# Kernel optimization log

Hardware: AMD Instinct MI355X
Metric: run time of the kernel (lower is better)

The kernel has to match this reference:

```python
import jax, jax.numpy as jnp
import numpy as np

EPS = 1e-6

def _ln(x):
    m = jnp.mean(x, -1, keepdims=True)
    v = jnp.mean((x - m) ** 2, -1, keepdims=True)
    return (x - m) * jax.lax.rsqrt(v + EPS)

def _rms(x, w):
    return x * jax.lax.rsqrt(jnp.mean(x * x, -1, keepdims=True) + EPS) * w

def _rotate_half(x):
    xr = x.reshape(x.shape[:-1] + (-1, 2))
    return jnp.stack([-xr[..., 1], xr[..., 0]], axis=-1).reshape(x.shape)

def _rope(x, cos, sin):
    # x: [B,L,H,D]; cos/sin: [L,D] interleaved-duplicated per pair
    c = cos[None, :, None, :]
    s = sin[None, :, None, :]
    return x * c + _rotate_half(x) * s

def _modulate(x, shift, scale):
    return x * (1.0 + scale[:, None, :]) + shift[:, None, :]

def _gate(x, g):
    return x * g[:, None, :]

def setup_inputs() -> dict:
    key = jax.random.key(0)
    ks = jax.random.split(key, 20)
    B, LI, LT, D, NH, HD, M = 1, 2048, 256, 2048, 16, 128, 8192
    def n(k, shape, s=1.0):
        return jax.random.normal(k, shape, dtype=jnp.float32) * s
    theta = jax.random.uniform(ks[0], (LI, HD // 2), dtype=jnp.float32) * 6.2831853
    freqs_cos = jnp.repeat(jnp.cos(theta), 2, axis=-1)  # [LI, HD]
    freqs_sin = jnp.repeat(jnp.sin(theta), 2, axis=-1)
    inp = {
        'img': n(ks[1], (B, LI, D)),
        'txt': n(ks[2], (B, LT, D)),
        'vec': n(ks[3], (B, D)),
        'freqs_cos': freqs_cos,
        'freqs_sin': freqs_sin,
        'attn_mask': jnp.ones((B, LI + LT), dtype=bool),
        # img stream params
        'img_mod_w': n(ks[4], (D, 6 * D), 0.02), 'img_mod_b': jnp.zeros((6 * D,), jnp.float32),
        'img_qkv_w': n(ks[5], (D, 3 * D), 0.02),
        'img_qn_w': jnp.ones((HD,), jnp.float32), 'img_kn_w': jnp.ones((HD,), jnp.float32),
        'img_proj_w': n(ks[6], (D, D), 0.02),
        'img_fc1_w': n(ks[7], (D, M), 0.02), 'img_fc1_b': jnp.zeros((M,), jnp.float32),
        'img_fc2_w': n(ks[8], (M, D), 0.02), 'img_fc2_b': jnp.zeros((D,), jnp.float32),
        # txt stream params
        'txt_mod_w': n(ks[9], (D, 6 * D), 0.02), 'txt_mod_b': jnp.zeros((6 * D,), jnp.float32),
        'txt_qkv_w': n(ks[10], (D, 3 * D), 0.02),
        'txt_qn_w': jnp.ones((HD,), jnp.float32), 'txt_kn_w': jnp.ones((HD,), jnp.float32),
        'txt_proj_w': n(ks[11], (D, D), 0.02),
        'txt_fc1_w': n(ks[12], (D, M), 0.02), 'txt_fc1_b': jnp.zeros((M,), jnp.float32),
        'txt_fc2_w': n(ks[13], (M, D), 0.02), 'txt_fc2_b': jnp.zeros((D,), jnp.float32),
    }
    return inp

def reference(img, txt, vec, freqs_cos, freqs_sin, attn_mask,
              img_mod_w, img_mod_b, img_qkv_w, img_qn_w, img_kn_w, img_proj_w,
              img_fc1_w, img_fc1_b, img_fc2_w, img_fc2_b,
              txt_mod_w, txt_mod_b, txt_qkv_w, txt_qn_w, txt_kn_w, txt_proj_w,
              txt_fc1_w, txt_fc1_b, txt_fc2_w, txt_fc2_b):
    B, LI, D = img.shape
    LT = txt.shape[1]
    HD = img_qn_w.shape[0]
    NH = D // HD
    vec_s = jax.nn.silu(vec)
    im = vec_s @ img_mod_w + img_mod_b
    i_s1, i_sc1, i_g1, i_s2, i_sc2, i_g2 = jnp.split(im, 6, axis=-1)
    tm = vec_s @ txt_mod_w + txt_mod_b
    t_s1, t_sc1, t_g1, t_s2, t_sc2, t_g2 = jnp.split(tm, 6, axis=-1)
    # img pre-attention
    ix = _modulate(_ln(img), i_s1, i_sc1)
    iqkv = (ix @ img_qkv_w).reshape(B, LI, 3, NH, HD)
    iq = _rms(iqkv[:, :, 0], img_qn_w)
    ik = _rms(iqkv[:, :, 1], img_kn_w)
    iv = iqkv[:, :, 2]
    iq = _rope(iq, freqs_cos, freqs_sin)
    ik = _rope(ik, freqs_cos, freqs_sin)
    # txt pre-attention (no rope)
    tx = _modulate(_ln(txt), t_s1, t_sc1)
    tqkv = (tx @ txt_qkv_w).reshape(B, LT, 3, NH, HD)
    tq = _rms(tqkv[:, :, 0], txt_qn_w)
    tk = _rms(tqkv[:, :, 1], txt_kn_w)
    tv = tqkv[:, :, 2]
    # joint attention over concat(img, txt)
    q = jnp.concatenate([iq, tq], axis=1)  # [B,S,H,D]
    k = jnp.concatenate([ik, tk], axis=1)
    v = jnp.concatenate([iv, tv], axis=1)
    scores = jnp.einsum('bqhd,bkhd->bhqk', q, k) / jnp.sqrt(jnp.float32(HD))
    scores = jnp.where(attn_mask[:, None, None, :], scores, jnp.float32(-1e30))
    p = jax.nn.softmax(scores, axis=-1)
    attn = jnp.einsum('bhqk,bkhd->bqhd', p, v).reshape(B, LI + LT, D)
    img_attn, txt_attn = attn[:, :LI], attn[:, LI:]
    # img residual branches
    img = img + _gate(img_attn @ img_proj_w, i_g1)
    h = _modulate(_ln(img), i_s2, i_sc2)
    h = jax.nn.gelu(h @ img_fc1_w + img_fc1_b, approximate=True) @ img_fc2_w + img_fc2_b
    img = img + _gate(h, i_g2)
    # txt residual branches
    txt = txt + _gate(txt_attn @ txt_proj_w, t_g1)
    h = _modulate(_ln(txt), t_s2, t_sc2)
    h = jax.nn.gelu(h @ txt_fc1_w + txt_fc1_b, approximate=True) @ txt_fc2_w + txt_fc2_b
    txt = txt + _gate(h, t_g2)
    return (img, txt)
```

## Files before the change

### kernel.cpp

```cpp
#include <hip/hip_runtime.h>
#include <hip/hip_bf16.h>
#include <cstdint>
#include <cstddef>

typedef __bf16 bf16x8 __attribute__((ext_vector_type(8)));
typedef float  f32x4  __attribute__((ext_vector_type(4)));
typedef __hip_bfloat16 hbf16;

#define DEVI static __device__ __forceinline__

DEVI unsigned short f2bf_bits(float x){
  hbf16 h = __float2bfloat16(x);
  return *reinterpret_cast<unsigned short*>(&h);
}
DEVI float gelu_tanh(float x){
  float u = x*(1.0f + 0.044715f*x*x);
  float t = exp2f(-2.3022119f*u);
  return x/(1.0f+t);
}

typedef __attribute__((address_space(1))) const unsigned int* gas_p;
typedef __attribute__((address_space(3))) unsigned int* las_p;
DEVI void gload16(const void* g, void* l){
  __builtin_amdgcn_global_load_lds((gas_p)g, (las_p)l, 16, 0, 0);
}


__global__ void silu_k(const float* __restrict__ v, float* __restrict__ o, int n){
  int i = blockIdx.x*blockDim.x + threadIdx.x;
  if (i < n){ float x = v[i]; o[i] = x/(1.0f+__expf(-x)); }
}

__global__ __launch_bounds__(256) void mod_part_k(const float* __restrict__ vs,
                                                  const float* __restrict__ W,
                                                  float* __restrict__ part){
  int j  = blockIdx.x*1024 + threadIdx.x*4;
  int i0 = blockIdx.y*64;
  float4 acc = {0.f,0.f,0.f,0.f};
  for (int i=0;i<64;i++){
    float s = vs[i0+i];
    float4 w = *(const float4*)(W + (size_t)(i0+i)*12288 + j);
    acc.x += s*w.x; acc.y += s*w.y; acc.z += s*w.z; acc.w += s*w.w;
  }
  *(float4*)(part + (size_t)blockIdx.y*12288 + j) = acc;
}

__global__ __launch_bounds__(256) void mod_red_k(const float* __restrict__ part,
                                                 const float* __restrict__ b,
                                                 float* __restrict__ out){
  int j = blockIdx.x*1024 + threadIdx.x*4;
  float4 acc = *(const float4*)(b + j);
  #pragma unroll
  for (int y=0;y<32;y++){
    float4 p = *(const float4*)(part + (size_t)y*12288 + j);
    acc.x += p.x; acc.y += p.y; acc.z += p.z; acc.w += p.w;
  }
  *(float4*)(out + j) = acc;
}

__global__ __launch_bounds__(256) void ln_mod_k(
    const float* __restrict__ Xi, const float* __restrict__ Xt,
    const float* __restrict__ sh_i, const float* __restrict__ sc_i,
    const float* __restrict__ sh_t, const float* __restrict__ sc_t,
    hbf16* __restrict__ Yi, hbf16* __restrict__ Yt){
  __shared__ float red[8];
  const int row = blockIdx.x, tid = threadIdx.x;
  const float* X; const float* sh; const float* sc; hbf16* Y; int r;
  if (row < 2048){ X = Xi; sh = sh_i; sc = sc_i; Y = Yi; r = row; }
  else           { X = Xt; sh = sh_t; sc = sc_t; Y = Yt; r = row - 2048; }
  const float* x = X + (size_t)r*2048;
  float4 a = *(const float4*)(x + tid*8);
  float4 c = *(const float4*)(x + tid*8 + 4);
  float s  = a.x+a.y+a.z+a.w + c.x+c.y+c.z+c.w;
  float s2 = a.x*a.x+a.y*a.y+a.z*a.z+a.w*a.w + c.x*c.x+c.y*c.y+c.z*c.z+c.w*c.w;
  #pragma unroll
  for (int m=1;m<64;m<<=1){ s += __shfl_xor(s,m,64); s2 += __shfl_xor(s2,m,64); }
  if ((tid&63)==0){ red[tid>>6] = s; red[4+(tid>>6)] = s2; }
  __syncthreads();
  float S  = red[0]+red[1]+red[2]+red[3];
  float S2 = red[4]+red[5]+red[6]+red[7];
  float mean = S*(1.f/2048.f);
  float var  = S2*(1.f/2048.f) - mean*mean;
  float rs = rsqrtf(var + 1e-6f);
  float xv[8] = {a.x,a.y,a.z,a.w,c.x,c.y,c.z,c.w};
  #pragma unroll
  for (int j=0;j<8;j++){
    int n = tid*8 + j;
    float yv = (xv[j]-mean)*rs*(1.f+sc[n]) + sh[n];
    Y[(size_t)r*2048 + n] = __float2bfloat16(yv);
  }
}

__global__ __launch_bounds__(256) void transp3_k(const float* __restrict__ W1,
                                                 hbf16* __restrict__ Wt1,
                                                 const float* __restrict__ W2,
                                                 hbf16* __restrict__ Wt2,
                                                 int K, int N){
  const float* W = blockIdx.z ? W2 : W1;
  hbf16* Wt = blockIdx.z ? Wt2 : Wt1;
  __shared__ float tile[128][68];
  const int n0 = blockIdx.x*64, k0 = blockIdx.y*128;
  const int tid = threadIdx.x;
  #pragma unroll
  for (int i=0;i<8;i++){
    int c = i*256 + tid;
    int k = c>>4, nq = c&15;
    float4 v = *(const float4*)(W + (size_t)(k0+k)*N + n0 + nq*4);
    *(float4*)&tile[k][nq*4] = v;
  }
  __syncthreads();
  const int n = tid>>2, kseg = tid&3;
  unsigned short buf[32];
  #pragma unroll
  for (int j=0;j<32;j++) buf[j] = f2bf_bits(tile[kseg*32+j][n]);
  hbf16* dst = Wt + (size_t)(n0+n)*K + k0 + kseg*32;
  *(uint4*)(dst)      = *(const uint4*)&buf[0];
  *(uint4*)(dst + 8)  = *(const uint4*)&buf[8];
  *(uint4*)(dst + 16) = *(const uint4*)&buf[16];
  *(uint4*)(dst + 24) = *(const uint4*)&buf[24];
}

__global__ __launch_bounds__(256) void vtransp_k(const hbf16* __restrict__ V,
                                                 hbf16* __restrict__ Vt){
  __shared__ unsigned short tile[64][72];
  const int t0 = blockIdx.x*64, d0 = blockIdx.y*64;
  const int tid = threadIdx.x;
  #pragma unroll
  for (int i=0;i<2;i++){
    int c = i*256 + tid, row = c>>3, jj = c&7;
    uint4 v = *(const uint4*)(V + (size_t)(t0+row)*2048 + d0 + jj*8);
    *(uint4*)&tile[row][jj*8] = v;
  }
  __syncthreads();
  const int d = tid>>2, seg = tid&3;
  unsigned short buf[16];
  #pragma unroll
  for (int j=0;j<16;j++) buf[j] = tile[seg*16+j][d];
  *(uint4*)(Vt + (size_t)(d0+d)*2304 + t0 + seg*16)     = *(const uint4*)&buf[0];
  *(uint4*)(Vt + (size_t)(d0+d)*2304 + t0 + seg*16 + 8) = *(const uint4*)&buf[8];
}

template<int EPI>
__global__ __launch_bounds__(256,4) void gemm_k(
    const hbf16* __restrict__ A1, const hbf16* __restrict__ B1,
    float* __restrict__ Cf1, hbf16* __restrict__ Cb1,
    const float* __restrict__ bias1, const float* __restrict__ gate1,
    const float* __restrict__ res1,
    const hbf16* __restrict__ A2, const hbf16* __restrict__ B2,
    float* __restrict__ Cf2, hbf16* __restrict__ Cb2,
    const float* __restrict__ bias2, const float* __restrict__ gate2,
    const float* __restrict__ res2,
    int nbx, int nby1, int nby2, int N, int K)
{
  __shared__ unsigned short As[128*64];
  __shared__ unsigned short Bs[128*64];
  const int tid = threadIdx.x;
  const int wv = tid>>6, ln = tid&63;
  const int nwg = nbx*(nby1+nby2), q = nwg>>3;
  const int w  = blockIdx.x;
  const int w2 = (w&7)*q + (w>>3);
  int n0, m0;
  const hbf16* A; const hbf16* Bt; float* Cf; hbf16* Cb;
  const float* bias; const float* gate; const float* res;
  if (w2 < nbx*nby1){
    n0 = (w2/nby1)*128; m0 = (w2%nby1)*128;
    A=A1; Bt=B1; Cf=Cf1; Cb=Cb1; bias=bias1; gate=gate1; res=res1;
  } else {
    int w3 = w2 - nbx*nby1;
    n0 = (w3/nby2)*128; m0 = (w3%nby2)*128;
    A=A2; Bt=B2; Cf=Cf2; Cb=Cb2; bias=bias2; gate=gate2; res=res2;
  }
  const int wm = (wv>>1)*64, wn = (wv&1)*64;
  f32x4 acc[4][4];
  #pragma unroll
  for (int i=0;i<4;i++)
    #pragma unroll
    for (int j=0;j<4;j++) acc[i][j] = (f32x4){0.f,0.f,0.f,0.f};

  const int lrow = ln>>3;
  const int jsrc = (ln&7) ^ lrow;
  const int NT = K>>6;

  for (int kt=0; kt<NT; ++kt){
    const int kk = kt<<6;
    #pragma unroll
    for (int j=0;j<4;j++){
      int row = wv*32 + j*8 + lrow;
      gload16(A  + (size_t)(m0+row)*K + kk + jsrc*8, &As[(wv*4+j)*512]);
      gload16(Bt + (size_t)(n0+row)*K + kk + jsrc*8, &Bs[(wv*4+j)*512]);
    }
    __syncthreads();
    #pragma unroll
    for (int ks=0; ks<2; ++ks){
      bf16x8 af[4], bfv[4];
      #pragma unroll
      for (int qq=0;qq<4;qq++){
        int row = wm + qq*16 + (ln&15);
        int jj  = ks*4 + (ln>>4);
        af[qq] = *(const bf16x8*)&As[row*64 + ((jj^(row&7))<<3)];
      }
      #pragma unroll
      for (int qq=0;qq<4;qq++){
        int row = wn + qq*16 + (ln&15);
        int jj  = ks*4 + (ln>>4);
        bfv[qq] = *(const bf16x8*)&Bs[row*64 + ((jj^(row&7))<<3)];
      }
      #pragma unroll
      for (int i=0;i<4;i++)
        #pragma unroll
        for (int j=0;j<4;j++)
          acc[i][j] = __builtin_amdgcn_mfma_f32_16x16x32_bf16(af[i], bfv[j], acc[i][j], 0,0,0);
    }
    __syncthreads();
  }
  #pragma unroll
  for (int i=0;i<4;i++){
    int mbase = m0 + wm + i*16 + ((ln>>4)<<2);
    #pragma unroll
    for (int j=0;j<4;j++){
      int n = n0 + wn + j*16 + (ln&15);
      #pragma unroll
      for (int r=0;r<4;r++){
        size_t idx = (size_t)(mbase+r)*N + n;
        float v = acc[i][j][r];
        if constexpr (EPI==0){ Cf[idx] = v; }
        else if constexpr (EPI==1){ Cb[idx] = __float2bfloat16(gelu_tanh(v + bias[n])); }
        else if constexpr (EPI==2){ Cf[idx] = res[idx] + gate[n]*v; }
        else if constexpr (EPI==3){ Cf[idx] = res[idx] + gate[n]*(v + bias[n]); }
        else { Cb[idx] = __float2bfloat16(v); }
      }
    }
  }
}

__global__ __launch_bounds__(256,4) void gemmqkv_k(
    const hbf16* __restrict__ A1, const hbf16* __restrict__ B1,
    const float* __restrict__ qn1, const float* __restrict__ kn1,
    int tok1, int rope1,
    const hbf16* __restrict__ A2, const hbf16* __restrict__ B2,
    const float* __restrict__ qn2, const float* __restrict__ kn2,
    int tok2, int rope2,
    const float* __restrict__ fcos_, const float* __restrict__ fsin_,
    hbf16* __restrict__ qb, hbf16* __restrict__ kb, hbf16* __restrict__ vb,
    int nbx, int nby1, int nby2, int K)
{
  __shared__ unsigned short As[128*64];
  __shared__ unsigned short Bs[128*64];
  __shared__ float ssb[2][128];
  const int tid = threadIdx.x;
  const int wv = tid>>6, ln = tid&63;
  const int nwg = nbx*(nby1+nby2), q = nwg>>3;
  const int w  = blockIdx.x;
  const int w2 = (w&7)*q + (w>>3);
  int n0, m0, tok, dorope;
  const hbf16* A; const hbf16* Bt; const float* qn; const float* kn;
  if (w2 < nbx*nby1){
    n0 = (w2/nby1)*128; m0 = (w2%nby1)*128;
    A=A1; Bt=B1; qn=qn1; kn=kn1; tok=tok1; dorope=rope1;
  } else {
    int w3 = w2 - nbx*nby1;
    n0 = (w3/nby2)*128; m0 = (w3%nby2)*128;
    A=A2; Bt=B2; qn=qn2; kn=kn2; tok=tok2; dorope=rope2;
  }
  const int wm = (wv>>1)*64, wn = (wv&1)*64;
  const int lm = ln&15, lk = ln>>4;
  f32x4 acc[4][4];
  #pragma unroll
  for (int i=0;i<4;i++)
    #pragma unroll
    for (int j=0;j<4;j++) acc[i][j] = (f32x4){0.f,0.f,0.f,0.f};

  const int lrow = ln>>3;
  const int jsrc = (ln&7) ^ lrow;
  const int NT = K>>6;

  for (int kt=0; kt<NT; ++kt){
    const int kk = kt<<6;
    #pragma unroll
    for (int j=0;j<4;j++){
      int row = wv*32 + j*8 + lrow;
      gload16(A  + (size_t)(m0+row)*K + kk + jsrc*8, &As[(wv*4+j)*512]);
      gload16(Bt + (size_t)(n0+row)*K + kk + jsrc*8, &Bs[(wv*4+j)*512]);
    }
    __syncthreads();
    #pragma unroll
    for (int ks=0; ks<2; ++ks){
      bf16x8 af[4], bfv[4];
      #pragma unroll
      for (int qq=0;qq<4;qq++){
        int row = wm + qq*16 + lm;
        int jj  = ks*4 + lk;
        af[qq] = *(const bf16x8*)&As[row*64 + ((jj^(row&7))<<3)];
      }
      #pragma unroll
      for (int qq=0;qq<4;qq++){
        int row = wn + qq*16 + lm;
        int jj  = ks*4 + lk;
        bfv[qq] = *(const bf16x8*)&Bs[row*64 + ((jj^(row&7))<<3)];
      }
      #pragma unroll
      for (int i=0;i<4;i++)
        #pragma unroll
        for (int j=0;j<4;j++)
          acc[i][j] = __builtin_amdgcn_mfma_f32_16x16x32_bf16(af[i], bfv[j], acc[i][j], 0,0,0);
    }
    __syncthreads();
  }

  const int which = n0 >> 11;
  const int head  = (n0 >> 7) & 15;
  if (which == 2){
    #pragma unroll
    for (int i=0;i<4;i++){
      int mbase = m0 + wm + i*16 + (lk<<2);
      #pragma unroll
      for (int j=0;j<4;j++){
        int d = wn + j*16 + lm;
        #pragma unroll
        for (int r=0;r<4;r++)
          vb[(size_t)(tok + mbase + r)*2048 + head*128 + d] = __float2bfloat16(acc[i][j][r]);
      }
    }
  } else {
    #pragma unroll
    for (int i=0;i<4;i++){
      #pragma unroll
      for (int r=0;r<4;r++){
        float p = 0.f;
        #pragma unroll
        for (int j=0;j<4;j++) p += acc[i][j][r]*acc[i][j][r];
        #pragma unroll
        for (int msk=1; msk<16; msk<<=1) p += __shfl_xor(p, msk, 64);
        if (lm == 0) ssb[wv&1][wm + i*16 + (lk<<2) + r] = p;
      }
    }
    __syncthreads();
    const float* wgt = (which==0) ? qn : kn;
    const float qs = (which==0) ? 0.12751745f : 1.0f;
    hbf16* outb = (which==0) ? qb : kb;
    #pragma unroll
    for (int i=0;i<4;i++){
      #pragma unroll
      for (int r=0;r<4;r++){
        int row = wm + i*16 + (lk<<2) + r;
        float ss = ssb[0][row] + ssb[1][row];
        float rs = rsqrtf(ss*(1.f/128.f) + 1e-6f) * qs;
        int t = m0 + row;
        #pragma unroll
        for (int j=0;j<4;j++){
          int d = wn + j*16 + lm;
          float z = acc[i][j][r]*rs*wgt[d];
          float out;
          float zp = __shfl_xor(z, 1, 64);
          if (dorope){
            float c = fcos_[(size_t)t*128 + d];
            float s = fsin_[(size_t)t*128 + d];
            out = ((d&1)==0) ? (z*c - zp*s) : (z*c + zp*s);
          } else out = z;
          outb[(size_t)(tok + t)*2048 + head*128 + d] = __float2bfloat16(out);
        }
      }
    }
  }
}

__global__ __launch_bounds__(512,4) void attn_k(
    const hbf16* __restrict__ Qg, const hbf16* __restrict__ Kg,
    const hbf16* __restrict__ Vtg, hbf16* __restrict__ sop01,
    hbf16* __restrict__ sop23, float* __restrict__ mlp)
{
  const int w = blockIdx.x;
  const int h = w & 15, quarter = (w>>4)&3, q0 = (w>>6)*128;
  const int tid = threadIdx.x, wv = tid>>6, ln = tid&63;
  __shared__ unsigned short Ks[2][64*128];
  __shared__ unsigned short Vs[2][128*64];
  __shared__ unsigned short Ps[8][16*64];

  bf16x8 qf[4];
  {
    const hbf16* qrow = Qg + (size_t)(q0 + wv*16 + (ln&15))*2048 + h*128 + (ln>>4)*8;
    #pragma unroll
    for (int ks=0;ks<4;ks++) qf[ks] = *(const bf16x8*)(qrow + ks*32);
  }

  f32x4 so[8];
  #pragma unroll
  for (int i=0;i<8;i++) so[i] = (f32x4){0.f,0.f,0.f,0.f};
  float m_run[4] = {-3e38f,-3e38f,-3e38f,-3e38f};
  float l_run[4] = {0.f,0.f,0.f,0.f};

  auto stage = [&](int buf, int kt){
    const int k0 = kt*64;
    #pragma unroll
    for (int i=0;i<2;i++){
      int c = i*512 + tid;
      int row = c>>4, jj = c&15;
      int js = jj ^ (row&7);
      gload16(Kg + (size_t)(k0+row)*2048 + h*128 + js*8, &Ks[buf][(i*512 + wv*64)*8]);
    }
    #pragma unroll
    for (int i=0;i<2;i++){
      int c = i*512 + tid;
      int row = c>>3, jj = c&7;
      int js = jj ^ (row&7);
      gload16(Vtg + (size_t)(h*128+row)*2304 + k0 + js*8, &Vs[buf][(i*512 + wv*64)*8]);
    }
  };

  const int t0 = quarter*9;
  stage(0, t0);
  __syncthreads();

  for (int it=0; it<9; ++it){
    const int cur = it&1;
    if (it+1 < 9) stage(cur^1, t0+it+1);

    f32x4 s[4];
    #pragma unroll
    for (int nb=0;nb<4;nb++) s[nb] = (f32x4){0.f,0.f,0.f,0.f};
    __builtin_amdgcn_s_setprio(1);
    #pragma unroll
    for (int ks=0;ks<4;ks++){
      #pragma unroll
      for (int nb=0;nb<4;nb++){
        int rk = nb*16 + (ln&15);
        int jq = ks*4 + (ln>>4);
        bf16x8 bk = *(const bf16x8*)&Ks[cur][rk*128 + ((jq^(rk&7))<<3)];
        s[nb] = __builtin_amdgcn_mfma_f32_16x16x32_bf16(qf[ks], bk, s[nb], 0,0,0);
      }
    }
    __builtin_amdgcn_s_setprio(0);

    float scl[4];
    #pragma unroll
    for (int r=0;r<4;r++){
      float m1 = fmaxf(fmaxf(s[0][r], s[1][r]), fmaxf(s[2][r], s[3][r]));
      #pragma unroll
      for (int msk=1; msk<16; msk<<=1) m1 = fmaxf(m1, __shfl_xor(m1, msk, 64));
      float mn = fmaxf(m_run[r], m1);
      scl[r] = exp2f(m_run[r] - mn);
      m_run[r] = mn;
    }
    #pragma unroll
    for (int nb=0;nb<4;nb++)
      #pragma unroll
      for (int r=0;r<4;r++)
        s[nb][r] = exp2f(s[nb][r] - m_run[r]);
    #pragma unroll
    for (int r=0;r<4;r++){
      float sm = s[0][r]+s[1][r]+s[2][r]+s[3][r];
      #pragma unroll
      for (int msk=1; msk<16; msk<<=1) sm += __shfl_xor(sm, msk, 64);
      l_run[r] = l_run[r]*scl[r] + sm;
    }
    #pragma unroll
    for (int nb2=0;nb2<8;nb2++)
      #pragma unroll
      for (int r=0;r<4;r++) so[nb2][r] *= scl[r];

    #pragma unroll
    for (int nb=0;nb<4;nb++)
      #pragma unroll
      for (int r=0;r<4;r++){
        int m = ((ln>>4)<<2) + r;
        int n = nb*16 + (ln&15);
        Ps[wv][m*64 + (((n>>3)^(m&7))<<3) + (n&7)] = f2bf_bits(s[nb][r]);
      }

    __builtin_amdgcn_s_setprio(1);
    #pragma unroll
    for (int ks=0;ks<2;ks++){
      int mrow = ln&15;
      bf16x8 pa = *(const bf16x8*)&Ps[wv][mrow*64 + (((ks*4+(ln>>4))^(mrow&7))<<3)];
      #pragma unroll
      for (int nb2=0;nb2<8;nb2++){
        int rv = nb2*16 + (ln&15);
        int jv = ks*4 + (ln>>4);
        bf16x8 bv = *(const bf16x8*)&Vs[cur][rv*64 + ((jv^(rv&7))<<3)];
        so[nb2] = __builtin_amdgcn_mfma_f32_16x16x32_bf16(pa, bv, so[nb2], 0,0,0);
      }
    }
    __builtin_amdgcn_s_setprio(0);
    __syncthreads();
  }

  hbf16* sbase = (quarter < 2 ? sop01 + (size_t)quarter*2304*2048
                              : sop23 + (size_t)(quarter-2)*2304*2048);
  #pragma unroll
  for (int r=0;r<4;r++){
    int m = q0 + wv*16 + ((ln>>4)<<2) + r;
    #pragma unroll
    for (int nb2=0;nb2<8;nb2++){
      int d = h*128 + nb2*16 + (ln&15);
      sbase[(size_t)m*2048 + d] = __float2bfloat16(so[nb2][r]);
    }
  }
  if ((ln&15)==0){
    #pragma unroll
    for (int r=0;r<4;r++){
      int m = q0 + wv*16 + ((ln>>4)<<2) + r;
      float* p = mlp + ((size_t)(quarter*2304 + m)*16 + h)*2;
      p[0] = m_run[r]; p[1] = l_run[r];
    }
  }
}

__global__ __launch_bounds__(256) void amerge_k(const hbf16* __restrict__ sop01,
                                                const hbf16* __restrict__ sop23,
                                                const float* __restrict__ mlp,
                                                hbf16* __restrict__ Og){
  const int q = blockIdx.x, tid = threadIdx.x;
  const int d0 = tid*8, h = tid>>4;
  float mv[4], lv[4];
  float m = -3e38f;
  #pragma unroll
  for (int h4=0;h4<4;h4++){
    const float* p = mlp + ((size_t)(h4*2304 + q)*16 + h)*2;
    mv[h4] = p[0]; lv[h4] = p[1];
    m = fmaxf(m, mv[h4]);
  }
  float wgt[4], den = 0.f;
  #pragma unroll
  for (int h4=0;h4<4;h4++){ wgt[h4] = exp2f(mv[h4]-m); den += wgt[h4]*lv[h4]; }
  float inv = 1.0f/den;
  float acc[8] = {0,0,0,0,0,0,0,0};
  #pragma unroll
  for (int h4=0;h4<4;h4++){
    const hbf16* s = (h4<2 ? sop01 + (size_t)h4*2304*2048
                           : sop23 + (size_t)(h4-2)*2304*2048) + (size_t)q*2048 + d0;
    bf16x8 v = *(const bf16x8*)s;
    #pragma unroll
    for (int j=0;j<8;j++) acc[j] += wgt[h4]*(float)v[j];
  }
  hbf16* o = Og + (size_t)q*2048 + d0;
  #pragma unroll
  for (int j=0;j<8;j++) o[j] = __float2bfloat16(acc[j]*inv);
}


extern "C" void kernel_launch(void* const* d_in, const int* in_sizes, int n_in,
                              void* d_out, int out_size, void* d_ws, size_t ws_size,
                              hipStream_t stream) {
  (void)in_sizes; (void)n_in; (void)out_size; (void)ws_size;
  const float* img   = (const float*)d_in[0];
  const float* txt   = (const float*)d_in[1];
  const float* vec   = (const float*)d_in[2];
  const float* fcos  = (const float*)d_in[3];
  const float* fsin  = (const float*)d_in[4];
  const float* img_mod_w = (const float*)d_in[6];
  const float* img_mod_b = (const float*)d_in[7];
  const float* img_qkv_w = (const float*)d_in[8];
  const float* img_qn_w  = (const float*)d_in[9];
  const float* img_kn_w  = (const float*)d_in[10];
  const float* img_proj_w= (const float*)d_in[11];
  const float* img_fc1_w = (const float*)d_in[12];
  const float* img_fc1_b = (const float*)d_in[13];
  const float* img_fc2_w = (const float*)d_in[14];
  const float* img_fc2_b = (const float*)d_in[15];
  const float* txt_mod_w = (const float*)d_in[16];
  const float* txt_mod_b = (const float*)d_in[17];
  const float* txt_qkv_w = (const float*)d_in[18];
  const float* txt_qn_w  = (const float*)d_in[19];
  const float* txt_kn_w  = (const float*)d_in[20];
  const float* txt_proj_w= (const float*)d_in[21];
  const float* txt_fc1_w = (const float*)d_in[22];
  const float* txt_fc1_b = (const float*)d_in[23];
  const float* txt_fc2_w = (const float*)d_in[24];
  const float* txt_fc2_b = (const float*)d_in[25];

  float* out_img = (float*)d_out;
  float* out_txt = out_img + (size_t)2048*2048;

  char* ws = (char*)d_ws;
  size_t off = 0;
  auto alloc = [&](size_t bytes)->void*{
    void* p = ws + off; off += (bytes + 255) & ~(size_t)255; return p;
  };
  hbf16* wt1     = (hbf16*)alloc((size_t)16777216*2);
  hbf16* wt2     = (hbf16*)alloc((size_t)16777216*2);
  float* vs      = (float*)alloc(2048*4);
  float* im      = (float*)alloc(12288*4);
  float* tm      = (float*)alloc(12288*4);
  float* part    = (float*)alloc((size_t)2*32*12288*4);
  hbf16* ix      = (hbf16*)alloc((size_t)2048*2048*2);
  hbf16* tx      = (hbf16*)alloc((size_t)256*2048*2);
  hbf16* iqkvb   = (hbf16*)alloc((size_t)2048*6144*2);
  hbf16* tqkvb   = (hbf16*)alloc((size_t)256*6144*2);
  hbf16* qb      = (hbf16*)alloc((size_t)2304*2048*2);
  hbf16* kb      = (hbf16*)alloc((size_t)2304*2048*2);
  hbf16* vb      = (hbf16*)alloc((size_t)2304*2048*2);
  hbf16* vtg     = (hbf16*)alloc((size_t)2048*2304*2);
  hbf16* attnb   = (hbf16*)alloc((size_t)2304*2048*2);
  float* img_mid = (float*)alloc((size_t)2048*2048*4);
  float* txt_mid = (float*)alloc((size_t)256*2048*4);
  hbf16* ix2     = (hbf16*)alloc((size_t)2048*2048*2);
  hbf16* tx2     = (hbf16*)alloc((size_t)256*2048*2);
  hbf16* h1i     = (hbf16*)alloc((size_t)2048*8192*2);
  hbf16* h1t     = (hbf16*)alloc((size_t)256*8192*2);
  float* mlp     = (float*)alloc((size_t)4*2304*16*2*4);
  (void)iqkvb; (void)tqkvb;
  hbf16* sop01 = (hbf16*)ix;
  hbf16* sop23 = (hbf16*)img_mid;

  silu_k<<<8,256,0,stream>>>(vec, vs, 2048);
  mod_part_k<<<dim3(12,32),256,0,stream>>>(vs, img_mod_w, part);
  mod_part_k<<<dim3(12,32),256,0,stream>>>(vs, txt_mod_w, part + (size_t)32*12288);
  mod_red_k<<<12,256,0,stream>>>(part, img_mod_b, im);
  mod_red_k<<<12,256,0,stream>>>(part + (size_t)32*12288, txt_mod_b, tm);

  ln_mod_k<<<2304,256,0,stream>>>(img, txt, im+0, im+2048, tm+0, tm+2048, ix, tx);

  transp3_k<<<dim3(96,16,2),256,0,stream>>>(img_qkv_w, wt1, txt_qkv_w, wt2, 2048, 6144);
  gemmqkv_k<<<864,256,0,stream>>>(ix, wt1, img_qn_w, img_kn_w, 0, 1,
                                  tx, wt2, txt_qn_w, txt_kn_w, 2048, 0,
                                  fcos, fsin, qb, kb, vb,
                                  48, 16, 2, 2048);

  vtransp_k<<<dim3(36,32),256,0,stream>>>(vb, vtg);

  attn_k<<<1152,512,0,stream>>>(qb, kb, vtg, sop01, sop23, mlp);
  amerge_k<<<2304,256,0,stream>>>(sop01, sop23, mlp, attnb);

  transp3_k<<<dim3(32,16,2),256,0,stream>>>(img_proj_w, wt1, txt_proj_w, wt2, 2048, 2048);
  gemm_k<2><<<288,256,0,stream>>>(attnb, wt1, img_mid, nullptr, nullptr, im+4096, img,
                                  attnb + (size_t)2048*2048, wt2, txt_mid, nullptr, nullptr, tm+4096, txt,
                                  16, 16, 2, 2048, 2048);

  ln_mod_k<<<2304,256,0,stream>>>(img_mid, txt_mid, im+6144, im+8192, tm+6144, tm+8192, ix2, tx2);

  transp3_k<<<dim3(128,16,2),256,0,stream>>>(img_fc1_w, wt1, txt_fc1_w, wt2, 2048, 8192);
  gemm_k<1><<<1152,256,0,stream>>>(ix2, wt1, nullptr, h1i, img_fc1_b, nullptr, nullptr,
                                   tx2, wt2, nullptr, h1t, txt_fc1_b, nullptr, nullptr,
                                   64, 16, 2, 8192, 2048);

  transp3_k<<<dim3(32,64,2),256,0,stream>>>(img_fc2_w, wt1, txt_fc2_w, wt2, 8192, 2048);
  gemm_k<3><<<288,256,0,stream>>>(h1i, wt1, out_img, nullptr, img_fc2_b, im+10240, img_mid,
                                  h1t, wt2, out_txt, nullptr, txt_fc2_b, tm+10240, txt_mid,
                                  16, 16, 2, 2048, 8192);
}
```

Baseline: 676.8 us.

## Use 256x128 tiles with 8-wave blocks for QKV and FC1 GEMMs

The QKV GEMM and the FC1 GEMM now use a 256-row by 128-column output tile per block, with 512 threads (8 waves) sharing one B tile, instead of 128x128 tiles with 4 waves. Fewer tiles means the weight tile is loaded from global memory fewer times overall. A new templated gemm256n_k kernel handles the FC1 GELU epilogue, and gemmqkv_k is adapted to the new indexing, including the RMS-norm partial-sum buffer. The cost is more LDS per block, fewer blocks in the grid, and the loss of the explicit occupancy hint of 4 blocks per CU.

```diff
diff --git a/kernel.cpp b/kernel.cpp
--- a/kernel.cpp
+++ b/kernel.cpp
@@ -233,7 +233,93 @@
   }
 }
 
-__global__ __launch_bounds__(256,4) void gemmqkv_k(
+template<int EPI>
+__global__ __launch_bounds__(512) void gemm256n_k(
+    const hbf16* __restrict__ A1, const hbf16* __restrict__ B1,
+    hbf16* __restrict__ Cb1, const float* __restrict__ bias1,
+    const hbf16* __restrict__ A2, const hbf16* __restrict__ B2,
+    hbf16* __restrict__ Cb2, const float* __restrict__ bias2,
+    int nbx, int nby1, int nby2, int N, int K)
+{
+  __shared__ unsigned short As[256*64];
+  __shared__ unsigned short Bs[128*64];
+  const int tid = threadIdx.x;
+  const int wv = tid>>6, ln = tid&63;
+  const int nwg = nbx*(nby1+nby2), q = nwg>>3;
+  const int w  = blockIdx.x;
+  const int w2 = (w&7)*q + (w>>3);
+  int n0, m0;
+  const hbf16* A; const hbf16* Bt; hbf16* Cb; const float* bias;
+  if (w2 < nbx*nby1){
+    n0 = (w2/nby1)*128; m0 = (w2%nby1)*256;
+    A=A1; Bt=B1; Cb=Cb1; bias=bias1;
+  } else {
+    int w3 = w2 - nbx*nby1;
+    n0 = (w3/nby2)*128; m0 = (w3%nby2)*256;
+    A=A2; Bt=B2; Cb=Cb2; bias=bias2;
+  }
+  const int wm = wv>>1, wn = wv&1;
+  const int lm = ln&15, lk = ln>>4;
+  f32x4 acc[4][4];
+  #pragma unroll
+  for (int i=0;i<4;i++)
+    #pragma unroll
+    for (int j=0;j<4;j++) acc[i][j] = (f32x4){0.f,0.f,0.f,0.f};
+
+  const int srow = tid>>3;
+  const int jsrc = (tid&7) ^ (srow&7);
+  const int NT = K>>6;
+
+  for (int kt=0; kt<NT; ++kt){
+    const int kk = kt<<6;
+    #pragma unroll
+    for (int i=0;i<4;i++)
+      gload16(A + (size_t)(m0 + i*64 + srow)*K + kk + jsrc*8, &As[(i*512+tid)*8]);
+    #pragma unroll
+    for (int i=0;i<2;i++)
+      gload16(Bt + (size_t)(n0 + i*64 + srow)*K + kk + jsrc*8, &Bs[(i*512+tid)*8]);
+    __syncthreads();
+    #pragma unroll
+    for (int ks=0; ks<2; ++ks){
+      bf16x8 af[4], bfv[4];
+      #pragma unroll
+      for (int qq=0;qq<4;qq++){
+        int row = wm*64 + qq*16 + lm;
+        int jj  = ks*4 + lk;
+        af[qq] = *(const bf16x8*)&As[row*64 + ((jj^(row&7))<<3)];
+      }
+      #pragma unroll
+      for (int qq=0;qq<4;qq++){
+        int row = wn*64 + qq*16 + lm;
+        int jj  = ks*4 + lk;
+        bfv[qq] = *(const bf16x8*)&Bs[row*64 + ((jj^(row&7))<<3)];
+      }
+      #pragma unroll
+      for (int i=0;i<4;i++)
+        #pragma unroll
+        for (int j=0;j<4;j++)
+          acc[i][j] = __builtin_amdgcn_mfma_f32_16x16x32_bf16(af[i], bfv[j], acc[i][j], 0,0,0);
+    }
+    __syncthreads();
+  }
+  #pragma unroll
+  for (int i=0;i<4;i++){
+    int mbase = m0 + wm*64 + i*16 + lk*4;
+    #pragma unroll
+    for (int j=0;j<4;j++){
+      int n = n0 + wn*64 + j*16 + lm;
+      #pragma unroll
+      for (int r=0;r<4;r++){
+        size_t idx = (size_t)(mbase+r)*N + n;
+        float v = acc[i][j][r];
+        if constexpr (EPI==1){ Cb[idx] = __float2bfloat16(gelu_tanh(v + bias[n])); }
+        else { Cb[idx] = __float2bfloat16(v); }
+      }
+    }
+  }
+}
+
+__global__ __launch_bounds__(512) void gemmqkv_k(
     const hbf16* __restrict__ A1, const hbf16* __restrict__ B1,
     const float* __restrict__ qn1, const float* __restrict__ kn1,
     int tok1, int rope1,
@@ -244,9 +330,9 @@
     hbf16* __restrict__ qb, hbf16* __restrict__ kb, hbf16* __restrict__ vb,
     int nbx, int nby1, int nby2, int K)
 {
-  __shared__ unsigned short As[128*64];
+  __shared__ unsigned short As[256*64];
   __shared__ unsigned short Bs[128*64];
-  __shared__ float ssb[2][128];
+  __shared__ float ssb[2][256];
   const int tid = threadIdx.x;
   const int wv = tid>>6, ln = tid&63;
   const int nwg = nbx*(nby1+nby2), q = nwg>>3;
@@ -255,14 +341,14 @@
   int n0, m0, tok, dorope;
   const hbf16* A; const hbf16* Bt; const float* qn; const float* kn;
   if (w2 < nbx*nby1){
-    n0 = (w2/nby1)*128; m0 = (w2%nby1)*128;
+    n0 = (w2/nby1)*128; m0 = (w2%nby1)*256;
     A=A1; Bt=B1; qn=qn1; kn=kn1; tok=tok1; dorope=rope1;
   } else {
     int w3 = w2 - nbx*nby1;
-    n0 = (w3/nby2)*128; m0 = (w3%nby2)*128;
+    n0 = (w3/nby2)*128; m0 = (w3%nby2)*256;
     A=A2; Bt=B2; qn=qn2; kn=kn2; tok=tok2; dorope=rope2;
   }
-  const int wm = (wv>>1)*64, wn = (wv&1)*64;
+  const int wm = wv>>1, wn = wv&1;
   const int lm = ln&15, lk = ln>>4;
   f32x4 acc[4][4];
   #pragma unroll
@@ -270,31 +356,31 @@
     #pragma unroll
     for (int j=0;j<4;j++) acc[i][j] = (f32x4){0.f,0.f,0.f,0.f};
 
-  const int lrow = ln>>3;
-  const int jsrc = (ln&7) ^ lrow;
+  const int srow = tid>>3;
+  const int jsrc = (tid&7) ^ (srow&7);
   const int NT = K>>6;
 
   for (int kt=0; kt<NT; ++kt){
     const int kk = kt<<6;
     #pragma unroll
-    for (int j=0;j<4;j++){
-      int row = wv*32 + j*8 + lrow;
-      gload16(A  + (size_t)(m0+row)*K + kk + jsrc*8, &As[(wv*4+j)*512]);
-      gload16(Bt + (size_t)(n0+row)*K + kk + jsrc*8, &Bs[(wv*4+j)*512]);
-    }
+    for (int i=0;i<4;i++)
+      gload16(A + (size_t)(m0 + i*64 + srow)*K + kk + jsrc*8, &As[(i*512+tid)*8]);
+    #pragma unroll
+    for (int i=0;i<2;i++)
+      gload16(Bt + (size_t)(n0 + i*64 + srow)*K + kk + jsrc*8, &Bs[(i*512+tid)*8]);
     __syncthreads();
     #pragma unroll
     for (int ks=0; ks<2; ++ks){
       bf16x8 af[4], bfv[4];
       #pragma unroll
       for (int qq=0;qq<4;qq++){
-        int row = wm + qq*16 + lm;
+        int row = wm*64 + qq*16 + lm;
         int jj  = ks*4 + lk;
         af[qq] = *(const bf16x8*)&As[row*64 + ((jj^(row&7))<<3)];
       }
       #pragma unroll
       for (int qq=0;qq<4;qq++){
-        int row = wn + qq*16 + lm;
+        int row = wn*64 + qq*16 + lm;
         int jj  = ks*4 + lk;
         bfv[qq] = *(const bf16x8*)&Bs[row*64 + ((jj^(row&7))<<3)];
       }
@@ -312,10 +398,10 @@
   if (which == 2){
     #pragma unroll
     for (int i=0;i<4;i++){
-      int mbase = m0 + wm + i*16 + (lk<<2);
+      int mbase = m0 + wm*64 + i*16 + lk*4;
       #pragma unroll
       for (int j=0;j<4;j++){
-        int d = wn + j*16 + lm;
+        int d = wn*64 + j*16 + lm;
         #pragma unroll
         for (int r=0;r<4;r++)
           vb[(size_t)(tok + mbase + r)*2048 + head*128 + d] = __float2bfloat16(acc[i][j][r]);
@@ -331,7 +417,7 @@
         for (int j=0;j<4;j++) p += acc[i][j][r]*acc[i][j][r];
         #pragma unroll
         for (int msk=1; msk<16; msk<<=1) p += __shfl_xor(p, msk, 64);
-        if (lm == 0) ssb[wv&1][wm + i*16 + (lk<<2) + r] = p;
+        if (lm == 0) ssb[wn][wm*64 + i*16 + lk*4 + r] = p;
       }
     }
     __syncthreads();
@@ -342,16 +428,16 @@
     for (int i=0;i<4;i++){
       #pragma unroll
       for (int r=0;r<4;r++){
-        int row = wm + i*16 + (lk<<2) + r;
+        int row = wm*64 + i*16 + lk*4 + r;
         float ss = ssb[0][row] + ssb[1][row];
         float rs = rsqrtf(ss*(1.f/128.f) + 1e-6f) * qs;
         int t = m0 + row;
         #pragma unroll
         for (int j=0;j<4;j++){
-          int d = wn + j*16 + lm;
+          int d = wn*64 + j*16 + lm;
           float z = acc[i][j][r]*rs*wgt[d];
+          float zp = __shfl_xor(z, 1, 64);
           float out;
-          float zp = __shfl_xor(z, 1, 64);
           if (dorope){
             float c = fcos_[(size_t)t*128 + d];
             float s = fsin_[(size_t)t*128 + d];
@@ -611,10 +697,10 @@
   ln_mod_k<<<2304,256,0,stream>>>(img, txt, im+0, im+2048, tm+0, tm+2048, ix, tx);
 
   transp3_k<<<dim3(96,16,2),256,0,stream>>>(img_qkv_w, wt1, txt_qkv_w, wt2, 2048, 6144);
-  gemmqkv_k<<<864,256,0,stream>>>(ix, wt1, img_qn_w, img_kn_w, 0, 1,
+  gemmqkv_k<<<432,512,0,stream>>>(ix, wt1, img_qn_w, img_kn_w, 0, 1,
                                   tx, wt2, txt_qn_w, txt_kn_w, 2048, 0,
                                   fcos, fsin, qb, kb, vb,
-                                  48, 16, 2, 2048);
+                                  48, 8, 1, 2048);
 
   vtransp_k<<<dim3(36,32),256,0,stream>>>(vb, vtg);
 
@@ -629,9 +715,9 @@
   ln_mod_k<<<2304,256,0,stream>>>(img_mid, txt_mid, im+6144, im+8192, tm+6144, tm+8192, ix2, tx2);
 
   transp3_k<<<dim3(128,16,2),256,0,stream>>>(img_fc1_w, wt1, txt_fc1_w, wt2, 2048, 8192);
-  gemm_k<1><<<1152,256,0,stream>>>(ix2, wt1, nullptr, h1i, img_fc1_b, nullptr, nullptr,
-                                   tx2, wt2, nullptr, h1t, txt_fc1_b, nullptr, nullptr,
-                                   64, 16, 2, 8192, 2048);
+  gemm256n_k<1><<<576,512,0,stream>>>(ix2, wt1, h1i, img_fc1_b,
+                                      tx2, wt2, h1t, txt_fc1_b,
+                                      64, 8, 1, 8192, 2048);
 
   transp3_k<<<dim3(32,64,2),256,0,stream>>>(img_fc2_w, wt1, txt_fc2_w, wt2, 8192, 2048);
   gemm_k<3><<<288,256,0,stream>>>(h1i, wt1, out_img, nullptr, img_fc2_b, im+10240, img_mid,
```

Result: no change. 690.2 us (+2.0%).
